# Performance work log

Hardware: AMD Instinct MI355X
Metric: run time of the kernel (lower is better)

Reference implementation:

```python
import jax, jax.numpy as jnp
import numpy as np

D = 256
H = 8
DH = D // H
N = 100000
B = 256
T = 131072
HID_FUSE = 256   # fuse MLP hidden = d_model
HID_HEAD = 256   # QuantileHeads hidden
NQ = 3           # quantiles (q10, q50, q90)


def setup_inputs() -> dict:
    key = jax.random.key(0)
    ks = jax.random.split(key, 32)
    p = lambda k, *s: (0.02 * jax.random.normal(k, s, dtype=jnp.float32))
    inp = {
        'node_embeddings': jax.random.normal(ks[0], (N, D), dtype=jnp.float32),
        'target_index': jax.random.randint(ks[1], (B,), 0, N),
        'port_index': jax.random.randint(ks[2], (T,), 0, N),
        'port_batch': jnp.sort(jax.random.randint(ks[3], (T,), 0, B)),
        'port_weight': jax.random.uniform(ks[4], (T,), dtype=jnp.float32),
        # PMA pooling params (learnable seed + MHA projections, no biases)
        'seed': p(ks[5], D),
        'Wq_p': p(ks[6], D, D), 'Wk_p': p(ks[7], D, D), 'Wv_p': p(ks[8], D, D), 'Wo_p': p(ks[9], D, D),
        # target->portfolio cross-attention params
        'Wq_c': p(ks[10], D, D), 'Wk_c': p(ks[11], D, D), 'Wv_c': p(ks[12], D, D), 'Wo_c': p(ks[13], D, D),
        # fuse LayerNorm(3d) + MLP
        'ln_g': jnp.ones((3 * D,), jnp.float32), 'ln_b': jnp.zeros((3 * D,), jnp.float32),
        'fuse_W1': p(ks[14], 3 * D, HID_FUSE), 'fuse_b1': jnp.zeros((HID_FUSE,), jnp.float32),
        'fuse_W2': p(ks[15], HID_FUSE, D), 'fuse_b2': jnp.zeros((D,), jnp.float32),
        # quantile heads MLP
        'head_W1': p(ks[16], D, HID_HEAD), 'head_b1': jnp.zeros((HID_HEAD,), jnp.float32),
        'head_W2': p(ks[17], HID_HEAD, NQ), 'head_b2': jnp.zeros((NQ,), jnp.float32),
    }
    return inp


def _segment_attend(logits, v, seg, num_segments):
    # logits [T,H], v [T,H,DH], seg [T] -> pooled [num_segments, H, DH]
    m = jax.ops.segment_max(logits, seg, num_segments=num_segments)  # [B,H]
    e = jnp.exp(logits - m[seg])                                      # [T,H]
    s = jax.ops.segment_sum(e, seg, num_segments=num_segments)        # [B,H]
    p = e / (s[seg] + 1e-9)
    return jax.ops.segment_sum(p[..., None] * v, seg, num_segments=num_segments)


def reference(node_embeddings, target_index, port_index, port_batch, port_weight,
              seed, Wq_p, Wk_p, Wv_p, Wo_p, Wq_c, Wk_c, Wv_c, Wo_c,
              ln_g, ln_b, fuse_W1, fuse_b1, fuse_W2, fuse_b2,
              head_W1, head_b1, head_W2, head_b2):
    b = target_index.shape[0]
    scale = float(DH) ** -0.5
    tgt = node_embeddings[target_index]          # [B,D]
    tok = node_embeddings[port_index]            # [T,D]
    logw = jnp.log(port_weight + 1e-8)           # DV01 weighting as logit bias

    # --- PMA: learnable seed query pools DV01-weighted portfolio tokens ---
    q_p = (seed @ Wq_p).reshape(H, DH)
    k_p = (tok @ Wk_p).reshape(-1, H, DH)
    v_p = (tok @ Wv_p).reshape(-1, H, DH)
    lg_p = jnp.einsum('thd,hd->th', k_p, q_p) * scale + logw[:, None]
    pooled = _segment_attend(lg_p, v_p, port_batch, b).reshape(b, D)
    contexts = pooled @ Wo_p                     # [B,D]; zeros for empty portfolios

    # --- target -> portfolio cross-attention (residual) ---
    q_c = (tgt @ Wq_c).reshape(b, H, DH)
    k_c = (tok @ Wk_c).reshape(-1, H, DH)
    v_c = (tok @ Wv_c).reshape(-1, H, DH)
    lg_c = jnp.einsum('thd,thd->th', k_c, q_c[port_batch]) * scale + logw[:, None]
    att = _segment_attend(lg_c, v_c, port_batch, b).reshape(b, D)
    fused = tgt + att @ Wo_c                     # [B,D]; == tgt for empty portfolios

    # --- fuse: concat -> LN -> MLP ---
    z = jnp.concatenate([tgt, contexts, fused], axis=-1)  # [B,3D]
    mu = jnp.mean(z, axis=-1, keepdims=True)
    var = jnp.var(z, axis=-1, keepdims=True)
    z = (z - mu) * jax.lax.rsqrt(var + 1e-5) * ln_g + ln_b
    z = jax.nn.relu(z @ fuse_W1 + fuse_b1) @ fuse_W2 + fuse_b2  # [B,D]

    # --- quantile heads ---
    out = jax.nn.relu(z @ head_W1 + head_b1) @ head_W2 + head_b2  # [B,NQ]
    return out
```

## Files before the change

### kernel.cpp

```cpp
#include <hip/hip_runtime.h>
#include <hip/hip_bf16.h>

typedef __attribute__((ext_vector_type(8))) short short8;
typedef __attribute__((ext_vector_type(4))) float floatx4;

#define SCALE 0.17677669529663687f

__device__ __forceinline__ unsigned short f2bf(float f) {
  unsigned int x = __float_as_uint(f);
  x += 0x7fffu + ((x >> 16) & 1u);
  return (unsigned short)(x >> 16);
}
__device__ __forceinline__ float bf2f(unsigned short u) {
  return __uint_as_float(((unsigned int)u) << 16);
}

__global__ __launch_bounds__(256) void k_qc_gemm(
    const float* __restrict__ node, const int* __restrict__ tgt_idx,
    const float* __restrict__ seed,
    const float* __restrict__ Wq_c, const float* __restrict__ Wq_p,
    float* __restrict__ q_all, int B)
{
  __shared__ float act_l[4 * 256];
  const int tid = threadIdx.x;
  const int bt = blockIdx.x, nt = blockIdx.y;
  const int BT = B >> 2;
  for (int i = tid; i < 4 * 256; i += 256) {
    int m = i >> 8, k = i & 255;
    int b = bt * 4 + m;
    float v = 0.f;
    if (b < B)       v = node[(size_t)tgt_idx[b] * 256 + k];
    else if (b == B) v = seed[k];
    act_l[i] = v;
  }
  __syncthreads();
  const float* W = (bt == BT) ? Wq_p : Wq_c;
  const int m = tid >> 6, lane = tid & 63, ks = lane >> 4, n = lane & 15;
  const int n0 = nt * 16;
  float acc = 0.f;
  const float* Wp = W + (size_t)(ks * 64) * 256 + n0 + n;
  const float* ap = &act_l[m * 256 + ks * 64];
  #pragma unroll 8
  for (int k = 0; k < 64; ++k) acc += ap[k] * Wp[(size_t)k * 256];
  acc += __shfl_xor(acc, 16, 64);
  acc += __shfl_xor(acc, 32, 64);
  const int b = bt * 4 + m;
  if (ks == 0 && b <= B) q_all[(size_t)b * 256 + n0 + n] = acc;
}

__global__ __launch_bounds__(256) void k_fold(
    const float* __restrict__ Wk_c, const float* __restrict__ Wk_p,
    const float* __restrict__ q_all, const int* __restrict__ port_batch,
    unsigned short* __restrict__ u_c_all, unsigned short* __restrict__ u_p_t,
    int* __restrict__ seg, int T, int B)
{
  const int tid = threadIdx.x;
  const int bt = blockIdx.x, dt = blockIdx.y;
  const int BT = B >> 2;
  if (dt == 0) {
    int key = -1;
    if (bt < BT) { if (tid < 4) key = bt * 4 + tid; }
    else if (tid == 0) key = B;
    if (key >= 0) {
      int lo = 0, hi = T;
      while (lo < hi) { int mid = (lo + hi) >> 1; if (port_batch[mid] < key) lo = mid + 1; else hi = mid; }
      seg[key] = lo;
    }
  }
  const int m = tid >> 6, lane = tid & 63;
  const int b = bt * 4 + m;
  if (b > B) return;
  const float* Wk = (b == B) ? Wk_p : Wk_c;
  const float* q = q_all + (size_t)b * 256;
  #pragma unroll
  for (int t2 = 0; t2 < 2; ++t2) {
    const int idx = t2 * 64 + lane;
    const int h = idx >> 4;
    const int d = dt * 16 + (idx & 15);
    float acc = 0.f;
    const float* wr = Wk + (size_t)d * 256 + h * 32;
    const float* qr = q + h * 32;
    #pragma unroll 8
    for (int j = 0; j < 32; ++j) acc += wr[j] * qr[j];
    unsigned short v = f2bf(acc);
    if (b < B) u_c_all[(size_t)b * 2048 + h * 256 + d] = v;
    else       u_p_t[h * 256 + d] = v;
  }
}

__global__ __launch_bounds__(256, 2) void attn_kernel(
    const float* __restrict__ node,
    const int* __restrict__ port_index,
    const float* __restrict__ port_weight,
    const unsigned short* __restrict__ u_p_t,
    const unsigned short* __restrict__ u_c_all,
    const int* __restrict__ seg,
    float* __restrict__ slabs, int T, int S)
{
  __shared__ __align__(16) unsigned short tok_lds[64 * 264];
  __shared__ __align__(16) unsigned short E_t[16 * 72];
  __shared__ float l_lds[16];

  const int tid  = threadIdx.x;
  const int s    = blockIdx.x;
  const int b    = blockIdx.y;
  const int lane = tid & 63;
  const int w    = tid >> 6;
  const int q    = lane >> 4;
  const int n    = lane & 15;

  if (tid < 16) l_lds[tid] = 0.f;

  short8 ufrag[8];
  const unsigned short* ubase = (n < 8) ? (u_p_t + n * 256)
                                        : (u_c_all + (size_t)b * 2048 + (n - 8) * 256);
  #pragma unroll
  for (int s8 = 0; s8 < 8; ++s8)
    ufrag[s8] = *(const short8*)(ubase + q * 8 + s8 * 32);

  const int start  = seg[b];
  const int end    = seg[b + 1];
  const int ntiles = (end - start + 63) >> 6;

  floatx4 sacc[4];
  #pragma unroll
  for (int nt = 0; nt < 4; ++nt) sacc[nt] = (floatx4){0.f, 0.f, 0.f, 0.f};

  __syncthreads();

  for (int it = s; it < ntiles; it += S) {
    const int tbase = start + it * 64;
    {
      int t0 = tbase + w * 16 + n;
      int idxv = port_index[t0 < T ? t0 : T - 1];
      #pragma unroll
      for (int i = 0; i < 16; ++i) {
        int rb = __shfl(idxv, i, 64);
        floatx4 v = *(const floatx4*)(node + (size_t)rb * 256 + lane * 4);
        unsigned int p0 = (unsigned int)f2bf(v[0]) | ((unsigned int)f2bf(v[1]) << 16);
        unsigned int p1 = (unsigned int)f2bf(v[2]) | ((unsigned int)f2bf(v[3]) << 16);
        uint2 pk; pk.x = p0; pk.y = p1;
        *(uint2*)(tok_lds + (w * 16 + i) * 264 + lane * 4) = pk;
      }
    }
    float pw[4];
    #pragma unroll
    for (int r = 0; r < 4; ++r) { int tr = tbase + w * 16 + q * 4 + r; pw[r] = port_weight[tr < T ? tr : T - 1]; }

    floatx4 lacc = (floatx4){0.f, 0.f, 0.f, 0.f};
    #pragma unroll
    for (int k = 0; k < 8; ++k) {
      short8 af = *(const short8*)(tok_lds + (w * 16 + n) * 264 + q * 8 + k * 32);
      lacc = __builtin_amdgcn_mfma_f32_16x16x32_bf16(af, ufrag[k], lacc, 0, 0, 0);
    }
    float lsum = 0.f;
    #pragma unroll
    for (int r = 0; r < 4; ++r) {
      const int tr = tbase + w * 16 + q * 4 + r;
      float e = 0.f;
      if (tr < end) {
        float lg = lacc[r] * SCALE + logf(pw[r] + 1e-8f);
        e = __expf(lg);
      }
      unsigned short eb = f2bf(e);
      E_t[n * 72 + w * 16 + q * 4 + r] = eb;
      lsum += bf2f(eb);
    }
    lsum += __shfl_xor(lsum, 16, 64);
    lsum += __shfl_xor(lsum, 32, 64);
    if (lane < 16) atomicAdd(&l_lds[lane], lsum);
    __syncthreads();
    short8 ea0 = *(const short8*)(E_t + n * 72 + q * 8);
    short8 ea1 = *(const short8*)(E_t + n * 72 + 32 + q * 8);
    #pragma unroll
    for (int nt = 0; nt < 4; ++nt) {
      const int dcol = w * 64 + nt * 16 + n;
      short8 b0, b1;
      #pragma unroll
      for (int j = 0; j < 8; ++j) b0[j] = (short)tok_lds[(q * 8 + j) * 264 + dcol];
      #pragma unroll
      for (int j = 0; j < 8; ++j) b1[j] = (short)tok_lds[(32 + q * 8 + j) * 264 + dcol];
      sacc[nt] = __builtin_amdgcn_mfma_f32_16x16x32_bf16(ea0, b0, sacc[nt], 0, 0, 0);
      sacc[nt] = __builtin_amdgcn_mfma_f32_16x16x32_bf16(ea1, b1, sacc[nt], 0, 0, 0);
    }
    __syncthreads();
  }

  float* stage = (float*)tok_lds;
  #pragma unroll
  for (int nt = 0; nt < 4; ++nt)
    #pragma unroll
    for (int r = 0; r < 4; ++r)
      stage[(q * 4 + r) * 256 + w * 64 + nt * 16 + n] = sacc[nt][r];
  __syncthreads();
  float* sl = slabs + ((size_t)b * S + s) * 4224;
  #pragma unroll
  for (int i = 0; i < 4; ++i) {
    const int row = i * 4 + w;
    const int c0 = (tid & 63) * 4;
    *(floatx4*)(sl + row * 256 + c0) = *(const floatx4*)(stage + row * 256 + c0);
  }
  if (tid < 16) sl[4096 + tid] = l_lds[tid];
}

__global__ __launch_bounds__(256) void k_slab_gemm(
    const float* __restrict__ slabs, int S,
    const float* __restrict__ Wv_p, const float* __restrict__ Wv_c,
    float* __restrict__ X)
{
  __shared__ float act_l[4 * 256];
  __shared__ float lsum[4];
  const int tid = threadIdx.x;
  const int bt = blockIdx.x, nt = blockIdx.y, z = blockIdx.z;
  const int head = nt >> 1;
  const int row = z * 8 + head;
  if (tid < 4) {
    const float* sl = slabs + (size_t)(bt * 4 + tid) * S * 4224;
    float l = 0.f;
    for (int s = 0; s < S; ++s) l += sl[s * 4224 + 4096 + row];
    lsum[tid] = 1.0f / (l + 1e-9f);
  }
  __syncthreads();
  for (int i = tid; i < 4 * 256; i += 256) {
    int m = i >> 8, k = i & 255;
    const float* sl = slabs + (size_t)(bt * 4 + m) * S * 4224;
    float sum = 0.f;
    for (int s = 0; s < S; ++s) sum += sl[s * 4224 + row * 256 + k];
    act_l[i] = sum * lsum[m];
  }
  __syncthreads();
  const int m = tid >> 6, lane = tid & 63, ks = lane >> 4, n = lane & 15;
  const int n0 = nt * 16;
  const float* W = z ? Wv_c : Wv_p;
  float acc = 0.f;
  const float* Wp = W + (size_t)(ks * 64) * 256 + n0 + n;
  const float* ap = &act_l[m * 256 + ks * 64];
  #pragma unroll 8
  for (int k = 0; k < 64; ++k) acc += ap[k] * Wp[(size_t)k * 256];
  acc += __shfl_xor(acc, 16, 64);
  acc += __shfl_xor(acc, 32, 64);
  if (ks == 0)
    X[(size_t)(bt * 4 + m) * 512 + z * 256 + n0 + n] = acc;
}

__global__ __launch_bounds__(256) void k_plain_gemm(
    const float* __restrict__ act, int act_ld,
    const float* __restrict__ W0, const float* __restrict__ W1,
    const float* __restrict__ bias0, const float* __restrict__ bias1,
    float* __restrict__ outp, int out_ld,
    int K, int relu)
{
  __shared__ float act_l[4 * 768];
  const int tid = threadIdx.x;
  const int bt = blockIdx.x, nt = blockIdx.y, z = blockIdx.z;
  const float* W = z ? W1 : W0;
  const float* bias = z ? bias1 : bias0;
  for (int i = tid; i < 4 * K; i += 256) {
    int m = i / K, k = i - m * K;
    act_l[m * K + k] = act[(size_t)(bt * 4 + m) * act_ld + z * K + k];
  }
  __syncthreads();
  const int m = tid >> 6, lane = tid & 63, ks = lane >> 4, n = lane & 15;
  const int n0 = nt * 16;
  const int Kq = K >> 2;
  float acc = 0.f;
  const float* Wp = W + (size_t)(ks * Kq) * 256 + n0 + n;
  const float* ap = &act_l[m * K + ks * Kq];
  #pragma unroll 8
  for (int k = 0; k < Kq; ++k) acc += ap[k] * Wp[(size_t)k * 256];
  acc += __shfl_xor(acc, 16, 64);
  acc += __shfl_xor(acc, 32, 64);
  if (ks == 0) {
    float v = acc + (bias ? bias[n0 + n] : 0.f);
    if (relu) v = fmaxf(v, 0.f);
    outp[(size_t)(bt * 4 + m) * out_ld + z * 256 + n0 + n] = v;
  }
}

__global__ __launch_bounds__(256) void k_ln_gemm(
    const float* __restrict__ node, const int* __restrict__ tgt_idx,
    const float* __restrict__ zbuf,
    const float* __restrict__ ln_g, const float* __restrict__ ln_b,
    const float* __restrict__ fuse_W1, const float* __restrict__ fuse_b1,
    float* __restrict__ h1)
{
  __shared__ float act_l[4 * 768];
  const int tid = threadIdx.x;
  const int bt = blockIdx.x, nt = blockIdx.y;
  for (int i = tid; i < 4 * 256; i += 256) {
    int m = i >> 8, k = i & 255;
    int b = bt * 4 + m;
    float tg = node[(size_t)tgt_idx[b] * 256 + k];
    float C  = zbuf[(size_t)b * 512 + k];
    float Fp = zbuf[(size_t)b * 512 + 256 + k];
    act_l[m * 768 + k]       = tg;
    act_l[m * 768 + 256 + k] = C;
    act_l[m * 768 + 512 + k] = tg + Fp;
  }
  __syncthreads();
  const int m = tid >> 6, lane = tid & 63;
  {
    float s = 0.f;
    for (int k = lane; k < 768; k += 64) s += act_l[m * 768 + k];
    #pragma unroll
    for (int o = 32; o >= 1; o >>= 1) s += __shfl_xor(s, o, 64);
    const float mu = s * (1.0f / 768.0f);
    float v = 0.f;
    for (int k = lane; k < 768; k += 64) { float d = act_l[m * 768 + k] - mu; v += d * d; }
    #pragma unroll
    for (int o = 32; o >= 1; o >>= 1) v += __shfl_xor(v, o, 64);
    const float rstd = 1.0f / sqrtf(v * (1.0f / 768.0f) + 1e-5f);
    for (int k = lane; k < 768; k += 64)
      act_l[m * 768 + k] = (act_l[m * 768 + k] - mu) * rstd * ln_g[k] + ln_b[k];
  }
  __syncthreads();
  const int ks = lane >> 4, n = lane & 15;
  const int n0 = nt * 16;
  float acc = 0.f;
  const float* Wp = fuse_W1 + (size_t)(ks * 192) * 256 + n0 + n;
  const float* ap = &act_l[m * 768 + ks * 192];
  #pragma unroll 8
  for (int k = 0; k < 192; ++k) acc += ap[k] * Wp[(size_t)k * 256];
  acc += __shfl_xor(acc, 16, 64);
  acc += __shfl_xor(acc, 32, 64);
  if (ks == 0)
    h1[(size_t)(bt * 4 + m) * 256 + n0 + n] = fmaxf(acc + fuse_b1[n0 + n], 0.f);
}

__global__ __launch_bounds__(256) void k_outhead(
    const float* __restrict__ hh, const float* __restrict__ head_W2,
    const float* __restrict__ head_b2, float* __restrict__ out)
{
  const int tid = threadIdx.x;
  const int m = tid >> 6, lane = tid & 63;
  const int b = blockIdx.x * 4 + m;
  float a0 = 0.f, a1 = 0.f, a2 = 0.f;
  for (int k = lane; k < 256; k += 64) {
    float h = hh[(size_t)b * 256 + k];
    a0 += h * head_W2[k * 3 + 0];
    a1 += h * head_W2[k * 3 + 1];
    a2 += h * head_W2[k * 3 + 2];
  }
  #pragma unroll
  for (int o = 32; o >= 1; o >>= 1) {
    a0 += __shfl_xor(a0, o, 64);
    a1 += __shfl_xor(a1, o, 64);
    a2 += __shfl_xor(a2, o, 64);
  }
  if (lane == 0) {
    out[b * 3 + 0] = a0 + head_b2[0];
    out[b * 3 + 1] = a1 + head_b2[1];
    out[b * 3 + 2] = a2 + head_b2[2];
  }
}

extern "C" void kernel_launch(void* const* d_in, const int* in_sizes, int n_in,
                              void* d_out, int out_size, void* d_ws, size_t ws_size,
                              hipStream_t stream) {
  const float* node        = (const float*)d_in[0];
  const int*   tgt_idx     = (const int*)d_in[1];
  const int*   port_index  = (const int*)d_in[2];
  const int*   port_batch  = (const int*)d_in[3];
  const float* port_weight = (const float*)d_in[4];
  const float* seed        = (const float*)d_in[5];
  const float* Wq_p = (const float*)d_in[6];
  const float* Wk_p = (const float*)d_in[7];
  const float* Wv_p = (const float*)d_in[8];
  const float* Wo_p = (const float*)d_in[9];
  const float* Wq_c = (const float*)d_in[10];
  const float* Wk_c = (const float*)d_in[11];
  const float* Wv_c = (const float*)d_in[12];
  const float* Wo_c = (const float*)d_in[13];
  const float* ln_g = (const float*)d_in[14];
  const float* ln_b = (const float*)d_in[15];
  const float* fuse_W1 = (const float*)d_in[16];
  const float* fuse_b1 = (const float*)d_in[17];
  const float* fuse_W2 = (const float*)d_in[18];
  const float* fuse_b2 = (const float*)d_in[19];
  const float* head_W1 = (const float*)d_in[20];
  const float* head_b1 = (const float*)d_in[21];
  const float* head_W2 = (const float*)d_in[22];
  const float* head_b2 = (const float*)d_in[23];

  const int B = in_sizes[1];
  const int T = in_sizes[2];

  char* ws = (char*)d_ws;
  unsigned short* u_p_t   = (unsigned short*)ws;
  int*            seg     = (int*)(ws + 4096);
  unsigned short* u_c_all = (unsigned short*)(ws + 8192);
  float* X    = (float*)(ws + 8192);
  float* zbuf = (float*)(ws + 8192 + (size_t)B * 2048);
  size_t slab_off = 8192 + (size_t)B * 4096;
  float* slabs = (float*)(ws + slab_off);
  float* h1 = slabs;
  float* z2 = h1 + (size_t)B * 256;
  float* hh = z2 + (size_t)B * 256;

  size_t per_slice = (size_t)B * 4224 * 4;
  int S = 1;
  if (ws_size > slab_off + per_slice) {
    size_t fit = (ws_size - slab_off - ((size_t)(B + 1) * 1024 + 4096)) / per_slice;
    S = (int)(fit < 1 ? 1 : (fit > 4 ? 4 : fit));
  }
  float* q_all = (float*)(ws + slab_off + (size_t)S * per_slice);

  const int BT = B / 4;

  k_qc_gemm<<<dim3(BT + 1, 16), 256, 0, stream>>>(node, tgt_idx, seed,
      Wq_c, Wq_p, q_all, B);
  k_fold<<<dim3(BT + 1, 16), 256, 0, stream>>>(Wk_c, Wk_p, q_all, port_batch,
      u_c_all, u_p_t, seg, T, B);
  attn_kernel<<<dim3(S, B), 256, 0, stream>>>(node, port_index, port_weight,
      u_p_t, u_c_all, seg, slabs, T, S);
  k_slab_gemm<<<dim3(BT, 16, 2), 256, 0, stream>>>(slabs, S, Wv_p, Wv_c, X);
  k_plain_gemm<<<dim3(BT, 16, 2), 256, 0, stream>>>(X, 512, Wo_p, Wo_c,
      nullptr, nullptr, zbuf, 512, 256, 0);
  k_ln_gemm<<<dim3(BT, 16), 256, 0, stream>>>(node, tgt_idx, zbuf,
      ln_g, ln_b, fuse_W1, fuse_b1, h1);
  k_plain_gemm<<<dim3(BT, 16, 1), 256, 0, stream>>>(h1, 256, fuse_W2, nullptr,
      fuse_b2, nullptr, z2, 256, 256, 0);
  k_plain_gemm<<<dim3(BT, 16, 1), 256, 0, stream>>>(z2, 256, head_W1, nullptr,
      head_b1, nullptr, hh, 256, 256, 1);
  k_outhead<<<BT, 256, 0, stream>>>(hh, head_W2, head_b2, (float*)d_out);
}
```

Before: 304.6 us.

## Fuse tail GEMM chain into one cooperative kernel; cheapen attention conversions

Six small tail launches (value projection, output projection, LayerNorm+MLP, head MLP and output head) are merged into one cooperative kernel, with grid-wide syncs between stages. This removes per-launch overhead and the gaps between dependent kernels. The attention kernel now packs bf16 with the hardware v_cvt_pk_bf16_f32 instruction, replaces exp(x+log(w)) with exp(x)*w to drop a log per element, and raises its occupancy hint to 3. The cooperative launch depends on all 1024 blocks being co-resident, and the new pack instruction may round differently from the old manual rounding.

```diff
diff --git a/kernel.cpp b/kernel.cpp
--- a/kernel.cpp
+++ b/kernel.cpp
@@ -1,5 +1,8 @@
 #include <hip/hip_runtime.h>
 #include <hip/hip_bf16.h>
+#include <hip/hip_cooperative_groups.h>
+
+namespace cg = cooperative_groups;
 
 typedef __attribute__((ext_vector_type(8))) short short8;
 typedef __attribute__((ext_vector_type(4))) float floatx4;
@@ -88,7 +91,7 @@
   }
 }
 
-__global__ __launch_bounds__(256, 2) void attn_kernel(
+__global__ __launch_bounds__(256, 3) void attn_kernel(
     const float* __restrict__ node,
     const int* __restrict__ port_index,
     const float* __restrict__ port_weight,
@@ -137,9 +140,9 @@
       for (int i = 0; i < 16; ++i) {
         int rb = __shfl(idxv, i, 64);
         floatx4 v = *(const floatx4*)(node + (size_t)rb * 256 + lane * 4);
-        unsigned int p0 = (unsigned int)f2bf(v[0]) | ((unsigned int)f2bf(v[1]) << 16);
-        unsigned int p1 = (unsigned int)f2bf(v[2]) | ((unsigned int)f2bf(v[3]) << 16);
-        uint2 pk; pk.x = p0; pk.y = p1;
+        uint2 pk;
+        asm("v_cvt_pk_bf16_f32 %0, %1, %2" : "=v"(pk.x) : "v"(v[0]), "v"(v[1]));
+        asm("v_cvt_pk_bf16_f32 %0, %1, %2" : "=v"(pk.y) : "v"(v[2]), "v"(v[3]));
         *(uint2*)(tok_lds + (w * 16 + i) * 264 + lane * 4) = pk;
       }
     }
@@ -159,8 +162,7 @@
       const int tr = tbase + w * 16 + q * 4 + r;
       float e = 0.f;
       if (tr < end) {
-        float lg = lacc[r] * SCALE + logf(pw[r] + 1e-8f);
-        e = __expf(lg);
+        e = __expf(lacc[r] * SCALE) * (pw[r] + 1e-8f);
       }
       unsigned short eb = f2bf(e);
       E_t[n * 72 + w * 16 + q * 4 + r] = eb;
@@ -203,154 +205,172 @@
   if (tid < 16) sl[4096 + tid] = l_lds[tid];
 }
 
-__global__ __launch_bounds__(256) void k_slab_gemm(
+__global__ __launch_bounds__(256, 4) void k_tail(
     const float* __restrict__ slabs, int S,
     const float* __restrict__ Wv_p, const float* __restrict__ Wv_c,
-    float* __restrict__ X)
+    const float* __restrict__ Wo_p, const float* __restrict__ Wo_c,
+    const float* __restrict__ node, const int* __restrict__ tgt_idx,
+    const float* __restrict__ ln_g, const float* __restrict__ ln_b,
+    const float* __restrict__ fuse_W1, const float* __restrict__ fuse_b1,
+    const float* __restrict__ fuse_W2, const float* __restrict__ fuse_b2,
+    const float* __restrict__ head_W1, const float* __restrict__ head_b1,
+    const float* __restrict__ head_W2, const float* __restrict__ head_b2,
+    float* __restrict__ X, float* __restrict__ zbuf,
+    float* __restrict__ h1, float* __restrict__ z2,
+    float* __restrict__ hh, float* __restrict__ out)
 {
-  __shared__ float act_l[4 * 256];
+  cg::grid_group gg = cg::this_grid();
+  __shared__ float act_l[4 * 768];
   __shared__ float lsum[4];
   const int tid = threadIdx.x;
-  const int bt = blockIdx.x, nt = blockIdx.y, z = blockIdx.z;
-  const int head = nt >> 1;
-  const int row = z * 8 + head;
-  if (tid < 4) {
-    const float* sl = slabs + (size_t)(bt * 4 + tid) * S * 4224;
-    float l = 0.f;
-    for (int s = 0; s < S; ++s) l += sl[s * 4224 + 4096 + row];
-    lsum[tid] = 1.0f / (l + 1e-9f);
-  }
-  __syncthreads();
-  for (int i = tid; i < 4 * 256; i += 256) {
-    int m = i >> 8, k = i & 255;
-    const float* sl = slabs + (size_t)(bt * 4 + m) * S * 4224;
-    float sum = 0.f;
-    for (int s = 0; s < S; ++s) sum += sl[s * 4224 + row * 256 + k];
-    act_l[i] = sum * lsum[m];
-  }
-  __syncthreads();
+  const int bt = blockIdx.x, nt = blockIdx.y;
   const int m = tid >> 6, lane = tid & 63, ks = lane >> 4, n = lane & 15;
   const int n0 = nt * 16;
-  const float* W = z ? Wv_c : Wv_p;
-  float acc = 0.f;
-  const float* Wp = W + (size_t)(ks * 64) * 256 + n0 + n;
-  const float* ap = &act_l[m * 256 + ks * 64];
-  #pragma unroll 8
-  for (int k = 0; k < 64; ++k) acc += ap[k] * Wp[(size_t)k * 256];
-  acc += __shfl_xor(acc, 16, 64);
-  acc += __shfl_xor(acc, 32, 64);
-  if (ks == 0)
-    X[(size_t)(bt * 4 + m) * 512 + z * 256 + n0 + n] = acc;
-}
-
-__global__ __launch_bounds__(256) void k_plain_gemm(
-    const float* __restrict__ act, int act_ld,
-    const float* __restrict__ W0, const float* __restrict__ W1,
-    const float* __restrict__ bias0, const float* __restrict__ bias1,
-    float* __restrict__ outp, int out_ld,
-    int K, int relu)
-{
-  __shared__ float act_l[4 * 768];
-  const int tid = threadIdx.x;
-  const int bt = blockIdx.x, nt = blockIdx.y, z = blockIdx.z;
-  const float* W = z ? W1 : W0;
-  const float* bias = z ? bias1 : bias0;
-  for (int i = tid; i < 4 * K; i += 256) {
-    int m = i / K, k = i - m * K;
-    act_l[m * K + k] = act[(size_t)(bt * 4 + m) * act_ld + z * K + k];
-  }
-  __syncthreads();
-  const int m = tid >> 6, lane = tid & 63, ks = lane >> 4, n = lane & 15;
-  const int n0 = nt * 16;
-  const int Kq = K >> 2;
-  float acc = 0.f;
-  const float* Wp = W + (size_t)(ks * Kq) * 256 + n0 + n;
-  const float* ap = &act_l[m * K + ks * Kq];
-  #pragma unroll 8
-  for (int k = 0; k < Kq; ++k) acc += ap[k] * Wp[(size_t)k * 256];
-  acc += __shfl_xor(acc, 16, 64);
-  acc += __shfl_xor(acc, 32, 64);
-  if (ks == 0) {
-    float v = acc + (bias ? bias[n0 + n] : 0.f);
-    if (relu) v = fmaxf(v, 0.f);
-    outp[(size_t)(bt * 4 + m) * out_ld + z * 256 + n0 + n] = v;
-  }
-}
-
-__global__ __launch_bounds__(256) void k_ln_gemm(
-    const float* __restrict__ node, const int* __restrict__ tgt_idx,
-    const float* __restrict__ zbuf,
-    const float* __restrict__ ln_g, const float* __restrict__ ln_b,
-    const float* __restrict__ fuse_W1, const float* __restrict__ fuse_b1,
-    float* __restrict__ h1)
-{
-  __shared__ float act_l[4 * 768];
-  const int tid = threadIdx.x;
-  const int bt = blockIdx.x, nt = blockIdx.y;
-  for (int i = tid; i < 4 * 256; i += 256) {
-    int m = i >> 8, k = i & 255;
-    int b = bt * 4 + m;
-    float tg = node[(size_t)tgt_idx[b] * 256 + k];
-    float C  = zbuf[(size_t)b * 512 + k];
-    float Fp = zbuf[(size_t)b * 512 + 256 + k];
-    act_l[m * 768 + k]       = tg;
-    act_l[m * 768 + 256 + k] = C;
-    act_l[m * 768 + 512 + k] = tg + Fp;
-  }
-  __syncthreads();
-  const int m = tid >> 6, lane = tid & 63;
+
+  #pragma unroll 1
+  for (int z = 0; z < 2; ++z) {
+    const int row = z * 8 + (nt >> 1);
+    if (tid < 4) {
+      const float* sl = slabs + (size_t)(bt * 4 + tid) * S * 4224;
+      float l = 0.f;
+      for (int s = 0; s < S; ++s) l += sl[s * 4224 + 4096 + row];
+      lsum[tid] = 1.0f / (l + 1e-9f);
+    }
+    __syncthreads();
+    for (int i = tid; i < 4 * 256; i += 256) {
+      int mm = i >> 8, k = i & 255;
+      const float* sl = slabs + (size_t)(bt * 4 + mm) * S * 4224;
+      float sum = 0.f;
+      for (int s = 0; s < S; ++s) sum += sl[s * 4224 + row * 256 + k];
+      act_l[i] = sum * lsum[mm];
+    }
+    __syncthreads();
+    const float* W = z ? Wv_c : Wv_p;
+    float acc = 0.f;
+    const float* Wp = W + (size_t)(ks * 64) * 256 + n0 + n;
+    const float* ap = &act_l[m * 256 + ks * 64];
+    #pragma unroll 8
+    for (int k = 0; k < 64; ++k) acc += ap[k] * Wp[(size_t)k * 256];
+    acc += __shfl_xor(acc, 16, 64);
+    acc += __shfl_xor(acc, 32, 64);
+    if (ks == 0) X[(size_t)(bt * 4 + m) * 512 + z * 256 + n0 + n] = acc;
+    __syncthreads();
+  }
+  gg.sync();
+
+  #pragma unroll 1
+  for (int z = 0; z < 2; ++z) {
+    for (int i = tid; i < 4 * 256; i += 256) {
+      int mm = i >> 8, k = i & 255;
+      act_l[i] = X[(size_t)(bt * 4 + mm) * 512 + z * 256 + k];
+    }
+    __syncthreads();
+    const float* W = z ? Wo_c : Wo_p;
+    float acc = 0.f;
+    const float* Wp = W + (size_t)(ks * 64) * 256 + n0 + n;
+    const float* ap = &act_l[m * 256 + ks * 64];
+    #pragma unroll 8
+    for (int k = 0; k < 64; ++k) acc += ap[k] * Wp[(size_t)k * 256];
+    acc += __shfl_xor(acc, 16, 64);
+    acc += __shfl_xor(acc, 32, 64);
+    if (ks == 0) zbuf[(size_t)(bt * 4 + m) * 512 + z * 256 + n0 + n] = acc;
+    __syncthreads();
+  }
+  gg.sync();
+
   {
-    float s = 0.f;
-    for (int k = lane; k < 768; k += 64) s += act_l[m * 768 + k];
-    #pragma unroll
-    for (int o = 32; o >= 1; o >>= 1) s += __shfl_xor(s, o, 64);
-    const float mu = s * (1.0f / 768.0f);
-    float v = 0.f;
-    for (int k = lane; k < 768; k += 64) { float d = act_l[m * 768 + k] - mu; v += d * d; }
-    #pragma unroll
-    for (int o = 32; o >= 1; o >>= 1) v += __shfl_xor(v, o, 64);
-    const float rstd = 1.0f / sqrtf(v * (1.0f / 768.0f) + 1e-5f);
+    for (int i = tid; i < 4 * 256; i += 256) {
+      int mm = i >> 8, k = i & 255;
+      int b = bt * 4 + mm;
+      float tg = node[(size_t)tgt_idx[b] * 256 + k];
+      float C  = zbuf[(size_t)b * 512 + k];
+      float Fp = zbuf[(size_t)b * 512 + 256 + k];
+      act_l[mm * 768 + k]       = tg;
+      act_l[mm * 768 + 256 + k] = C;
+      act_l[mm * 768 + 512 + k] = tg + Fp;
+    }
+    __syncthreads();
+    float sv = 0.f;
+    for (int k = lane; k < 768; k += 64) sv += act_l[m * 768 + k];
+    #pragma unroll
+    for (int o = 32; o >= 1; o >>= 1) sv += __shfl_xor(sv, o, 64);
+    const float mu = sv * (1.0f / 768.0f);
+    float vv = 0.f;
+    for (int k = lane; k < 768; k += 64) { float d = act_l[m * 768 + k] - mu; vv += d * d; }
+    #pragma unroll
+    for (int o = 32; o >= 1; o >>= 1) vv += __shfl_xor(vv, o, 64);
+    const float rstd = 1.0f / sqrtf(vv * (1.0f / 768.0f) + 1e-5f);
     for (int k = lane; k < 768; k += 64)
       act_l[m * 768 + k] = (act_l[m * 768 + k] - mu) * rstd * ln_g[k] + ln_b[k];
-  }
-  __syncthreads();
-  const int ks = lane >> 4, n = lane & 15;
-  const int n0 = nt * 16;
-  float acc = 0.f;
-  const float* Wp = fuse_W1 + (size_t)(ks * 192) * 256 + n0 + n;
-  const float* ap = &act_l[m * 768 + ks * 192];
-  #pragma unroll 8
-  for (int k = 0; k < 192; ++k) acc += ap[k] * Wp[(size_t)k * 256];
-  acc += __shfl_xor(acc, 16, 64);
-  acc += __shfl_xor(acc, 32, 64);
-  if (ks == 0)
-    h1[(size_t)(bt * 4 + m) * 256 + n0 + n] = fmaxf(acc + fuse_b1[n0 + n], 0.f);
-}
-
-__global__ __launch_bounds__(256) void k_outhead(
-    const float* __restrict__ hh, const float* __restrict__ head_W2,
-    const float* __restrict__ head_b2, float* __restrict__ out)
-{
-  const int tid = threadIdx.x;
-  const int m = tid >> 6, lane = tid & 63;
-  const int b = blockIdx.x * 4 + m;
-  float a0 = 0.f, a1 = 0.f, a2 = 0.f;
-  for (int k = lane; k < 256; k += 64) {
-    float h = hh[(size_t)b * 256 + k];
-    a0 += h * head_W2[k * 3 + 0];
-    a1 += h * head_W2[k * 3 + 1];
-    a2 += h * head_W2[k * 3 + 2];
-  }
-  #pragma unroll
-  for (int o = 32; o >= 1; o >>= 1) {
-    a0 += __shfl_xor(a0, o, 64);
-    a1 += __shfl_xor(a1, o, 64);
-    a2 += __shfl_xor(a2, o, 64);
-  }
-  if (lane == 0) {
-    out[b * 3 + 0] = a0 + head_b2[0];
-    out[b * 3 + 1] = a1 + head_b2[1];
-    out[b * 3 + 2] = a2 + head_b2[2];
+    __syncthreads();
+    float acc = 0.f;
+    const float* Wp = fuse_W1 + (size_t)(ks * 192) * 256 + n0 + n;
+    const float* ap = &act_l[m * 768 + ks * 192];
+    #pragma unroll 8
+    for (int k = 0; k < 192; ++k) acc += ap[k] * Wp[(size_t)k * 256];
+    acc += __shfl_xor(acc, 16, 64);
+    acc += __shfl_xor(acc, 32, 64);
+    if (ks == 0)
+      h1[(size_t)(bt * 4 + m) * 256 + n0 + n] = fmaxf(acc + fuse_b1[n0 + n], 0.f);
+  }
+  gg.sync();
+
+  {
+    for (int i = tid; i < 4 * 256; i += 256) {
+      int mm = i >> 8, k = i & 255;
+      act_l[i] = h1[(size_t)(bt * 4 + mm) * 256 + k];
+    }
+    __syncthreads();
+    float acc = 0.f;
+    const float* Wp = fuse_W2 + (size_t)(ks * 64) * 256 + n0 + n;
+    const float* ap = &act_l[m * 256 + ks * 64];
+    #pragma unroll 8
+    for (int k = 0; k < 64; ++k) acc += ap[k] * Wp[(size_t)k * 256];
+    acc += __shfl_xor(acc, 16, 64);
+    acc += __shfl_xor(acc, 32, 64);
+    if (ks == 0)
+      z2[(size_t)(bt * 4 + m) * 256 + n0 + n] = acc + fuse_b2[n0 + n];
+  }
+  gg.sync();
+
+  {
+    for (int i = tid; i < 4 * 256; i += 256) {
+      int mm = i >> 8, k = i & 255;
+      act_l[i] = z2[(size_t)(bt * 4 + mm) * 256 + k];
+    }
+    __syncthreads();
+    float acc = 0.f;
+    const float* Wp = head_W1 + (size_t)(ks * 64) * 256 + n0 + n;
+    const float* ap = &act_l[m * 256 + ks * 64];
+    #pragma unroll 8
+    for (int k = 0; k < 64; ++k) acc += ap[k] * Wp[(size_t)k * 256];
+    acc += __shfl_xor(acc, 16, 64);
+    acc += __shfl_xor(acc, 32, 64);
+    if (ks == 0)
+      hh[(size_t)(bt * 4 + m) * 256 + n0 + n] = fmaxf(acc + head_b1[n0 + n], 0.f);
+  }
+  gg.sync();
+
+  if (nt == 0) {
+    const int b = bt * 4 + m;
+    float a0 = 0.f, a1 = 0.f, a2 = 0.f;
+    for (int k = lane; k < 256; k += 64) {
+      float h = hh[(size_t)b * 256 + k];
+      a0 += h * head_W2[k * 3 + 0];
+      a1 += h * head_W2[k * 3 + 1];
+      a2 += h * head_W2[k * 3 + 2];
+    }
+    #pragma unroll
+    for (int o = 32; o >= 1; o >>= 1) {
+      a0 += __shfl_xor(a0, o, 64);
+      a1 += __shfl_xor(a1, o, 64);
+      a2 += __shfl_xor(a2, o, 64);
+    }
+    if (lane == 0) {
+      out[b * 3 + 0] = a0 + head_b2[0];
+      out[b * 3 + 1] = a1 + head_b2[1];
+      out[b * 3 + 2] = a2 + head_b2[2];
+    }
   }
 }
 
@@ -396,6 +416,7 @@
   float* h1 = slabs;
   float* z2 = h1 + (size_t)B * 256;
   float* hh = z2 + (size_t)B * 256;
+  float* outp = (float*)d_out;
 
   size_t per_slice = (size_t)B * 4224 * 4;
   int S = 1;
@@ -413,14 +434,20 @@
       u_c_all, u_p_t, seg, T, B);
   attn_kernel<<<dim3(S, B), 256, 0, stream>>>(node, port_index, port_weight,
       u_p_t, u_c_all, seg, slabs, T, S);
-  k_slab_gemm<<<dim3(BT, 16, 2), 256, 0, stream>>>(slabs, S, Wv_p, Wv_c, X);
-  k_plain_gemm<<<dim3(BT, 16, 2), 256, 0, stream>>>(X, 512, Wo_p, Wo_c,
-      nullptr, nullptr, zbuf, 512, 256, 0);
-  k_ln_gemm<<<dim3(BT, 16), 256, 0, stream>>>(node, tgt_idx, zbuf,
-      ln_g, ln_b, fuse_W1, fuse_b1, h1);
-  k_plain_gemm<<<dim3(BT, 16, 1), 256, 0, stream>>>(h1, 256, fuse_W2, nullptr,
-      fuse_b2, nullptr, z2, 256, 256, 0);
-  k_plain_gemm<<<dim3(BT, 16, 1), 256, 0, stream>>>(z2, 256, head_W1, nullptr,
-      head_b1, nullptr, hh, 256, 256, 1);
-  k_outhead<<<BT, 256, 0, stream>>>(hh, head_W2, head_b2, (float*)d_out);
-}
+
+  void* args[] = {
+      (void*)&slabs, (void*)&S,
+      (void*)&Wv_p, (void*)&Wv_c,
+      (void*)&Wo_p, (void*)&Wo_c,
+      (void*)&node, (void*)&tgt_idx,
+      (void*)&ln_g, (void*)&ln_b,
+      (void*)&fuse_W1, (void*)&fuse_b1,
+      (void*)&fuse_W2, (void*)&fuse_b2,
+      (void*)&head_W1, (void*)&head_b1,
+      (void*)&head_W2, (void*)&head_b2,
+      (void*)&X, (void*)&zbuf,
+      (void*)&h1, (void*)&z2, (void*)&hh, (void*)&outp
+  };
+  hipLaunchCooperativeKernel((const void*)k_tail, dim3(BT, 16), dim3(256),
+                             args, 0, stream);
+}
```

Measured after the change: 823.5 us. +170.3%, slower.
